# Kernel tuning notes

Measured on AMD Instinct MI355X. Metric: run time of the kernel, lower is better.

The kernel has to match this reference:

```python
import jax, jax.numpy as jnp
import numpy as np

NUM_HEADS = 4
EPS = 1e-5  # GroupNorm default eps


def setup_inputs() -> dict:
    key = jax.random.key(0)
    ks = jax.random.split(key, 4)
    B, T, C, H, W = 4, 8, 128, 96, 96
    x = jax.random.normal(ks[0], (B, T, C, H, W), jnp.float32)
    pos_enc = jax.random.normal(ks[1], (1, 16, C, 1, 1), jnp.float32) * 0.02
    norm_w = jnp.ones((C,), jnp.float32)
    norm_b = jnp.zeros((C,), jnp.float32)
    qkv_w = jax.random.normal(ks[2], (3 * C, C), jnp.float32) * (1.0 / np.sqrt(C))
    proj_w = jax.random.normal(ks[3], (C, C), jnp.float32) * (1.0 / np.sqrt(C))
    return {"x": x, "pos_enc": pos_enc, "norm_w": norm_w, "norm_b": norm_b,
            "qkv_w": qkv_w, "proj_w": proj_w}


def reference(x, pos_enc, norm_w, norm_b, qkv_w, proj_w):
    B, T, C, H, W = x.shape
    nh = NUM_HEADS
    hd = C // nh
    scale = hd ** -0.5

    x = x + pos_enc[:, :T]

    # GroupNorm(1, C): normalize over (C,H,W) per (B,T) sample, biased var
    mean = x.mean(axis=(2, 3, 4), keepdims=True)
    var = x.var(axis=(2, 3, 4), keepdims=True)
    xn = (x - mean) * jax.lax.rsqrt(var + EPS)
    xn = xn * norm_w[None, None, :, None, None] + norm_b[None, None, :, None, None]

    # 1x1 conv -> matmul over channel dim; d = 3C
    qkv = jnp.einsum('btchw,dc->btdhw', xn, qkv_w)
    qkv = qkv.reshape(B, T, 3, nh, hd, H, W)
    q, k, v = qkv[:, :, 0], qkv[:, :, 1], qkv[:, :, 2]  # [B,T,nh,hd,H,W]

    # per-pixel temporal attention: scores [B,nh,H,W,T,T]
    attn = jnp.einsum('btndhw,bsndhw->bnhwts', q, k) * scale
    attn = jax.nn.softmax(attn, axis=-1)

    # only the last query row is kept (out[..., -1, :] in the original)
    out = jnp.einsum('bnhws,bsndhw->bndhw', attn[..., -1, :], v)
    out = out.reshape(B, C, H, W)
    return jnp.einsum('bchw,dc->bdhw', out, proj_w)
```

## Files before the change

kernel.cpp:

```cpp
#include <hip/hip_runtime.h>
#include <math.h>

#define BB 4
#define TT 8
#define CC 128
#define HWW 9216
#define NPG 1179648.0f
#define EPS 1e-5f
#define SCALE 0.17677669529663687f

#define WS_PART 0
#define WS_A    8192
#define WS_B    12288

typedef __attribute__((ext_vector_type(4))) float f32x4;

__device__ __forceinline__ void gload16(const float* g, float* l) {
    __builtin_amdgcn_global_load_lds(
        (const __attribute__((address_space(1))) void*)g,
        (__attribute__((address_space(3))) void*)l,
        16, 0, 0);
}

__global__ __launch_bounds__(256) void stats_kernel(
    const float* __restrict__ x, const float* __restrict__ pe,
    float* __restrict__ part)
{
    const int bid = blockIdx.x;
    const int g = bid >> 7, c = bid & 127;
    const int t = g & 7;
    const int tid = threadIdx.x;
    const float pec = pe[t * CC + c];
    const float4* row = (const float4*)(x + ((size_t)g * CC + c) * HWW);
    float s1 = 0.f, s2 = 0.f;
    #pragma unroll
    for (int i = 0; i < 9; ++i) {
        float4 v = row[tid + i * 256];
        float a = v.x + pec, b = v.y + pec, cc2 = v.z + pec, d = v.w + pec;
        s1 += (a + b) + (cc2 + d);
        s2 += (a * a + b * b) + (cc2 * cc2 + d * d);
    }
    for (int off = 32; off; off >>= 1) {
        s1 += __shfl_down(s1, off);
        s2 += __shfl_down(s2, off);
    }
    __shared__ float red[8];
    const int wid = tid >> 6, lane = tid & 63;
    if (lane == 0) { red[wid] = s1; red[4 + wid] = s2; }
    __syncthreads();
    if (tid == 0) {
        part[bid * 2 + 0] = red[0] + red[1] + red[2] + red[3];
        part[bid * 2 + 1] = red[4] + red[5] + red[6] + red[7];
    }
}

__global__ __launch_bounds__(128) void finalize_kernel(
    const float* __restrict__ pe, const float* __restrict__ nw,
    const float* __restrict__ nb, float* ws)
{
    const int g = blockIdx.x;
    const int c = threadIdx.x;
    const float* part = ws + WS_PART + g * 256;
    float s1 = part[c * 2 + 0];
    float s2 = part[c * 2 + 1];
    for (int off = 32; off; off >>= 1) {
        s1 += __shfl_down(s1, off);
        s2 += __shfl_down(s2, off);
    }
    __shared__ float r[4];
    const int wid = c >> 6, lane = c & 63;
    if (lane == 0) { r[wid] = s1; r[2 + wid] = s2; }
    __syncthreads();
    const float inv = 1.0f / NPG;
    const float mean = (r[0] + r[1]) * inv;
    const float var  = (r[2] + r[3]) * inv - mean * mean;
    const float rstd = rsqrtf(var + EPS);
    const int t = g & 7;
    const float a = rstd * nw[c];
    ws[WS_A + g * CC + c] = a;
    ws[WS_B + g * CC + c] = (pe[t * CC + c] - mean) * a + nb[c];
}

__global__ __launch_bounds__(1024, 4) void fused6_kernel(
    const float* __restrict__ x, const float* __restrict__ ws,
    const float* __restrict__ qkv_w, const float* __restrict__ proj_w,
    float* __restrict__ out)
{
    __shared__ __align__(16) float bufA[CC * 64];
    __shared__ __align__(16) float bufB[CC * 64];

    const int tid  = threadIdx.x;
    const int lane = tid & 63;
    const int w    = tid >> 6;
    const int wu   = __builtin_amdgcn_readfirstlane(w);
    const int n    = wu >> 2;
    const int hq   = wu & 3;
    const int b    = blockIdx.y;
    const int hw0  = blockIdx.x * 64;

    const float* A = ws + WS_A;
    const float* B = ws + WS_B;

    const int rsub = lane >> 4, coff = (lane & 15) * 4;

    auto stage = [&](int t, float* dst) {
        const size_t gb = (size_t)((b * TT + t) * CC) * HWW + hw0 + coff;
        #pragma unroll
        for (int k = 0; k < 2; ++k) {
            const int r0 = wu * 8 + k * 4;
            gload16(x + gb + (size_t)(r0 + rsub) * HWW, dst + r0 * 64);
        }
    };

    float u[32];
    auto score_partial = [&](const float* buf, const float* At, const float* Bt) {
        float s0 = 0.f, s1 = 0.f, s2 = 0.f, s3 = 0.f;
        #pragma unroll
        for (int j = 0; j < 32; j += 4) {
            float x0 = fmaf(buf[(hq * 32 + j + 0) * 64 + lane], At[j + 0], Bt[j + 0]);
            float x1 = fmaf(buf[(hq * 32 + j + 1) * 64 + lane], At[j + 1], Bt[j + 1]);
            float x2 = fmaf(buf[(hq * 32 + j + 2) * 64 + lane], At[j + 2], Bt[j + 2]);
            float x3 = fmaf(buf[(hq * 32 + j + 3) * 64 + lane], At[j + 3], Bt[j + 3]);
            s0 = fmaf(u[j + 0], x0, s0);
            s1 = fmaf(u[j + 1], x1, s1);
            s2 = fmaf(u[j + 2], x2, s2);
            s3 = fmaf(u[j + 3], x3, s3);
        }
        return (s0 + s1) + (s2 + s3);
    };

    stage(7, bufA);
    __syncthreads();

    const int g7 = b * TT + 7;
    const float* A7 = A + g7 * CC;
    const float* B7 = B + g7 * CC;
    {
        const float* Wq = qkv_w + (n * 32 + hq * 8) * CC;
        float q7[8] = {0.f,0.f,0.f,0.f,0.f,0.f,0.f,0.f};
        for (int c0 = 0; c0 < CC; c0 += 8) {
            float xv[8];
            #pragma unroll
            for (int i = 0; i < 8; ++i)
                xv[i] = fmaf(bufA[(c0 + i) * 64 + lane], A7[c0 + i], B7[c0 + i]);
            #pragma unroll
            for (int d = 0; d < 8; ++d) {
                #pragma unroll
                for (int i = 0; i < 8; ++i)
                    q7[d] = fmaf(Wq[d * CC + c0 + i], xv[i], q7[d]);
            }
        }
        #pragma unroll
        for (int d = 0; d < 8; ++d)
            bufB[(n * 32 + hq * 8 + d) * 64 + lane] = q7[d];
    }
    __syncthreads();

    #pragma unroll
    for (int j = 0; j < 32; ++j) u[j] = 0.f;
    {
        const float* Wk = qkv_w + (CC + n * 32) * CC + hq * 32;
        for (int d = 0; d < 32; ++d) {
            const float qv = bufB[(n * 32 + d) * 64 + lane];
            #pragma unroll
            for (int j = 0; j < 32; ++j)
                u[j] = fmaf(Wk[d * CC + j], qv, u[j]);
        }
    }
    __syncthreads();

    float ps[8];
    stage(0, bufB);
    ps[7] = score_partial(bufA, A7 + hq * 32, B7 + hq * 32);
    __syncthreads();
    #pragma unroll
    for (int t = 0; t < 7; ++t) {
        const float* cur = (t & 1) ? bufA : bufB;
        float* oth = (t & 1) ? bufB : bufA;
        if (t < 6) stage(t + 1, oth);
        const float* At = A + (b * TT + t) * CC + hq * 32;
        const float* Bt = B + (b * TT + t) * CC + hq * 32;
        ps[t] = score_partial(cur, At, Bt);
        __syncthreads();
    }

    stage(0, bufB);
    #pragma unroll
    for (int t = 0; t < 8; ++t)
        bufA[(wu * 8 + t) * 64 + lane] = ps[t];
    __syncthreads();

    float wt[8];
    {
        float sreg[8];
        #pragma unroll
        for (int t = 0; t < 8; ++t)
            sreg[t] = (bufA[((n * 4 + 0) * 8 + t) * 64 + lane] +
                       bufA[((n * 4 + 1) * 8 + t) * 64 + lane]) +
                      (bufA[((n * 4 + 2) * 8 + t) * 64 + lane] +
                       bufA[((n * 4 + 3) * 8 + t) * 64 + lane]);
        float m = fmaxf(fmaxf(fmaxf(sreg[0], sreg[1]), fmaxf(sreg[2], sreg[3])),
                        fmaxf(fmaxf(sreg[4], sreg[5]), fmaxf(sreg[6], sreg[7])));
        float l = 0.f;
        #pragma unroll
        for (int t = 0; t < 8; ++t) { wt[t] = __expf((sreg[t] - m) * SCALE); l += wt[t]; }
        const float invl = 1.0f / l;
        #pragma unroll
        for (int t = 0; t < 8; ++t) wt[t] *= invl;
    }
    __syncthreads();

    float xb[32];
    #pragma unroll
    for (int j = 0; j < 32; ++j) xb[j] = 0.f;
    #pragma unroll
    for (int t = 0; t < 8; ++t) {
        const float* cur = (t & 1) ? bufA : bufB;
        float* oth = (t & 1) ? bufB : bufA;
        if (t < 7) stage(t + 1, oth);
        const float* At = A + (b * TT + t) * CC + hq * 32;
        const float* Bt = B + (b * TT + t) * CC + hq * 32;
        const float wc = wt[t];
        #pragma unroll
        for (int j = 0; j < 32; ++j) {
            float xv = fmaf(cur[(hq * 32 + j) * 64 + lane], At[j], Bt[j]);
            xb[j] = fmaf(xv, wc, xb[j]);
        }
        __syncthreads();
    }

    {
        const float* Wv = qkv_w + (2 * CC + n * 32) * CC + hq * 32;
        float vprev[8];
        #pragma unroll
        for (int gi = 0; gi < 4; ++gi) {
            float vp[8];
            #pragma unroll
            for (int d = 0; d < 8; ++d) {
                float s0 = 0.f, s1 = 0.f, s2 = 0.f, s3 = 0.f;
                const float* Wr = Wv + (gi * 8 + d) * CC;
                #pragma unroll
                for (int c = 0; c < 32; c += 4) {
                    s0 = fmaf(Wr[c + 0], xb[c + 0], s0);
                    s1 = fmaf(Wr[c + 1], xb[c + 1], s1);
                    s2 = fmaf(Wr[c + 2], xb[c + 2], s2);
                    s3 = fmaf(Wr[c + 3], xb[c + 3], s3);
                }
                vp[d] = (s0 + s1) + (s2 + s3);
            }
            if (hq == 1) {
                #pragma unroll
                for (int d = 0; d < 8; ++d)
                    bufB[(n * 32 + gi * 8 + d) * 64 + lane] = vp[d];
            }
            if (hq == 3) {
                #pragma unroll
                for (int d = 0; d < 8; ++d)
                    bufA[(n * 32 + gi * 8 + d) * 64 + lane] = vp[d];
            }
            if (gi > 0) {
                if (hq == 0) {
                    #pragma unroll
                    for (int d = 0; d < 8; ++d) {
                        const int r = (n * 32 + (gi - 1) * 8 + d) * 64 + lane;
                        bufB[r] += vprev[d];
                    }
                }
                if (hq == 2) {
                    #pragma unroll
                    for (int d = 0; d < 8; ++d) {
                        const int r = (n * 32 + (gi - 1) * 8 + d) * 64 + lane;
                        bufA[r] += vprev[d];
                    }
                }
            }
            #pragma unroll
            for (int d = 0; d < 8; ++d) vprev[d] = vp[d];
            __syncthreads();
        }
        if (hq == 0) {
            #pragma unroll
            for (int d = 0; d < 8; ++d)
                bufB[(n * 32 + 24 + d) * 64 + lane] += vprev[d];
        }
        if (hq == 2) {
            #pragma unroll
            for (int d = 0; d < 8; ++d)
                bufA[(n * 32 + 24 + d) * 64 + lane] += vprev[d];
        }
    }
    __syncthreads();

    float y[8];
    #pragma unroll
    for (int e = 0; e < 8; ++e) y[e] = 0.f;
    for (int c0 = 0; c0 < CC; c0 += 16) {
        float vv[16];
        #pragma unroll
        for (int i = 0; i < 16; ++i)
            vv[i] = bufB[(c0 + i) * 64 + lane] + bufA[(c0 + i) * 64 + lane];
        #pragma unroll
        for (int e = 0; e < 8; ++e) {
            const float* Pr = proj_w + (wu * 8 + e) * CC + c0;
            #pragma unroll
            for (int i = 0; i < 16; ++i)
                y[e] = fmaf(Pr[i], vv[i], y[e]);
        }
    }
    const size_t ob = (size_t)(b * CC + wu * 8) * HWW + hw0 + lane;
    #pragma unroll
    for (int e = 0; e < 8; ++e)
        out[ob + (size_t)e * HWW] = y[e];
}

extern "C" void kernel_launch(void* const* d_in, const int* in_sizes, int n_in,
                              void* d_out, int out_size, void* d_ws, size_t ws_size,
                              hipStream_t stream) {
    const float* x      = (const float*)d_in[0];
    const float* pe     = (const float*)d_in[1];
    const float* nw     = (const float*)d_in[2];
    const float* nb     = (const float*)d_in[3];
    const float* qkv_w  = (const float*)d_in[4];
    const float* proj_w = (const float*)d_in[5];
    float* out = (float*)d_out;
    float* ws  = (float*)d_ws;

    stats_kernel<<<4096, 256, 0, stream>>>(x, pe, ws + WS_PART);
    finalize_kernel<<<32, 128, 0, stream>>>(pe, nw, nb, ws);
    fused6_kernel<<<dim3(HWW / 64, BB), 1024, 0, stream>>>(x, ws, qkv_w, proj_w, out);
}
```

Measured before the change: 471.6 us.

## Stage x tiles through registers with normalization applied before LDS write

Replaces the direct global-to-LDS async loads with register-staged loads that apply the GroupNorm affine (per-channel a,b held in registers) before writing to shared memory. Consumers then read already-normalized values, removing repeated per-element fma and the scalar loads of A/B coefficients in the score and weighted-sum loops. Loads for tile t+2 are issued ahead so global latency overlaps compute, and the value-accumulation loop is re-pipelined by one step. Softmax switches from __expf to exp2f with a prescaled constant. The cost is more registers per thread and extra VGPR traffic through LDS writes instead of the DMA-style load path.

```diff
diff --git a/kernel.cpp b/kernel.cpp
--- a/kernel.cpp
+++ b/kernel.cpp
@@ -8,19 +8,13 @@
 #define NPG 1179648.0f
 #define EPS 1e-5f
 #define SCALE 0.17677669529663687f
+#define SCALE2 0.2550181765195206f
 
 #define WS_PART 0
 #define WS_A    8192
 #define WS_B    12288
 
 typedef __attribute__((ext_vector_type(4))) float f32x4;
-
-__device__ __forceinline__ void gload16(const float* g, float* l) {
-    __builtin_amdgcn_global_load_lds(
-        (const __attribute__((address_space(1))) void*)g,
-        (__attribute__((address_space(3))) void*)l,
-        16, 0, 0);
-}
 
 __global__ __launch_bounds__(256) void stats_kernel(
     const float* __restrict__ x, const float* __restrict__ pe,
@@ -81,7 +75,7 @@
     ws[WS_B + g * CC + c] = (pe[t * CC + c] - mean) * a + nb[c];
 }
 
-__global__ __launch_bounds__(1024, 4) void fused6_kernel(
+__global__ __launch_bounds__(1024, 4) void fused7_kernel(
     const float* __restrict__ x, const float* __restrict__ ws,
     const float* __restrict__ qkv_w, const float* __restrict__ proj_w,
     float* __restrict__ out)
@@ -98,43 +92,51 @@
     const int b    = blockIdx.y;
     const int hw0  = blockIdx.x * 64;
 
-    const float* A = ws + WS_A;
-    const float* B = ws + WS_B;
-
-    const int rsub = lane >> 4, coff = (lane & 15) * 4;
-
-    auto stage = [&](int t, float* dst) {
-        const size_t gb = (size_t)((b * TT + t) * CC) * HWW + hw0 + coff;
-        #pragma unroll
-        for (int k = 0; k < 2; ++k) {
-            const int r0 = wu * 8 + k * 4;
-            gload16(x + gb + (size_t)(r0 + rsub) * HWW, dst + r0 * 64);
-        }
+    const int r  = tid >> 3;
+    const int k8 = (tid & 7) * 8;
+
+    float ar[8], br[8];
+    #pragma unroll
+    for (int t = 0; t < 8; ++t) {
+        ar[t] = ws[WS_A + (b * TT + t) * CC + r];
+        br[t] = ws[WS_B + (b * TT + t) * CC + r];
+    }
+
+    const float* xrow = x + ((size_t)(b * TT) * CC + r) * HWW + hw0 + k8;
+
+    f32x4 rg0, rg1;
+    auto ldtile = [&](int t) {
+        const float* p = xrow + (size_t)t * CC * HWW;
+        rg0 = *(const f32x4*)(p);
+        rg1 = *(const f32x4*)(p + 4);
     };
+    auto wrtile = [&](float a, float bb2, float* dst) {
+        f32x4 f0, f1;
+        f0.x = fmaf(rg0.x, a, bb2); f0.y = fmaf(rg0.y, a, bb2);
+        f0.z = fmaf(rg0.z, a, bb2); f0.w = fmaf(rg0.w, a, bb2);
+        f1.x = fmaf(rg1.x, a, bb2); f1.y = fmaf(rg1.y, a, bb2);
+        f1.z = fmaf(rg1.z, a, bb2); f1.w = fmaf(rg1.w, a, bb2);
+        *(f32x4*)&dst[r * 64 + k8]     = f0;
+        *(f32x4*)&dst[r * 64 + k8 + 4] = f1;
+    };
 
     float u[32];
-    auto score_partial = [&](const float* buf, const float* At, const float* Bt) {
+    auto score = [&](const float* buf) {
         float s0 = 0.f, s1 = 0.f, s2 = 0.f, s3 = 0.f;
         #pragma unroll
         for (int j = 0; j < 32; j += 4) {
-            float x0 = fmaf(buf[(hq * 32 + j + 0) * 64 + lane], At[j + 0], Bt[j + 0]);
-            float x1 = fmaf(buf[(hq * 32 + j + 1) * 64 + lane], At[j + 1], Bt[j + 1]);
-            float x2 = fmaf(buf[(hq * 32 + j + 2) * 64 + lane], At[j + 2], Bt[j + 2]);
-            float x3 = fmaf(buf[(hq * 32 + j + 3) * 64 + lane], At[j + 3], Bt[j + 3]);
-            s0 = fmaf(u[j + 0], x0, s0);
-            s1 = fmaf(u[j + 1], x1, s1);
-            s2 = fmaf(u[j + 2], x2, s2);
-            s3 = fmaf(u[j + 3], x3, s3);
+            s0 = fmaf(u[j + 0], buf[(hq * 32 + j + 0) * 64 + lane], s0);
+            s1 = fmaf(u[j + 1], buf[(hq * 32 + j + 1) * 64 + lane], s1);
+            s2 = fmaf(u[j + 2], buf[(hq * 32 + j + 2) * 64 + lane], s2);
+            s3 = fmaf(u[j + 3], buf[(hq * 32 + j + 3) * 64 + lane], s3);
         }
         return (s0 + s1) + (s2 + s3);
     };
 
-    stage(7, bufA);
-    __syncthreads();
-
-    const int g7 = b * TT + 7;
-    const float* A7 = A + g7 * CC;
-    const float* B7 = B + g7 * CC;
+    ldtile(7);
+    wrtile(ar[7], br[7], bufA);
+    __syncthreads();
+
     {
         const float* Wq = qkv_w + (n * 32 + hq * 8) * CC;
         float q7[8] = {0.f,0.f,0.f,0.f,0.f,0.f,0.f,0.f};
@@ -142,7 +144,7 @@
             float xv[8];
             #pragma unroll
             for (int i = 0; i < 8; ++i)
-                xv[i] = fmaf(bufA[(c0 + i) * 64 + lane], A7[c0 + i], B7[c0 + i]);
+                xv[i] = bufA[(c0 + i) * 64 + lane];
             #pragma unroll
             for (int d = 0; d < 8; ++d) {
                 #pragma unroll
@@ -156,6 +158,8 @@
     }
     __syncthreads();
 
+    ldtile(0);
+
     #pragma unroll
     for (int j = 0; j < 32; ++j) u[j] = 0.f;
     {
@@ -170,21 +174,29 @@
     __syncthreads();
 
     float ps[8];
-    stage(0, bufB);
-    ps[7] = score_partial(bufA, A7 + hq * 32, B7 + hq * 32);
-    __syncthreads();
+    wrtile(ar[0], br[0], bufB);
+    ps[7] = score(bufA);
+    ldtile(1);
+    __syncthreads();
+
     #pragma unroll
     for (int t = 0; t < 7; ++t) {
-        const float* cur = (t & 1) ? bufA : bufB;
-        float* oth = (t & 1) ? bufB : bufA;
-        if (t < 6) stage(t + 1, oth);
-        const float* At = A + (b * TT + t) * CC + hq * 32;
-        const float* Bt = B + (b * TT + t) * CC + hq * 32;
-        ps[t] = score_partial(cur, At, Bt);
+        const float* curb = (t & 1) ? bufA : bufB;
+        float* othb = (t & 1) ? bufB : bufA;
+        if (t < 6) {
+            if (t == 0) wrtile(ar[1], br[1], othb);
+            if (t == 1) wrtile(ar[2], br[2], othb);
+            if (t == 2) wrtile(ar[3], br[3], othb);
+            if (t == 3) wrtile(ar[4], br[4], othb);
+            if (t == 4) wrtile(ar[5], br[5], othb);
+            if (t == 5) wrtile(ar[6], br[6], othb);
+        }
+        if (t < 5) ldtile(t + 2);
+        ps[t] = score(curb);
         __syncthreads();
     }
 
-    stage(0, bufB);
+    ldtile(0);
     #pragma unroll
     for (int t = 0; t < 8; ++t)
         bufA[(wu * 8 + t) * 64 + lane] = ps[t];
@@ -203,7 +215,7 @@
                         fmaxf(fmaxf(sreg[4], sreg[5]), fmaxf(sreg[6], sreg[7])));
         float l = 0.f;
         #pragma unroll
-        for (int t = 0; t < 8; ++t) { wt[t] = __expf((sreg[t] - m) * SCALE); l += wt[t]; }
+        for (int t = 0; t < 8; ++t) { wt[t] = exp2f((sreg[t] - m) * SCALE2); l += wt[t]; }
         const float invl = 1.0f / l;
         #pragma unroll
         for (int t = 0; t < 8; ++t) wt[t] *= invl;
@@ -215,19 +227,34 @@
     for (int j = 0; j < 32; ++j) xb[j] = 0.f;
     #pragma unroll
     for (int t = 0; t < 8; ++t) {
-        const float* cur = (t & 1) ? bufA : bufB;
-        float* oth = (t & 1) ? bufB : bufA;
-        if (t < 7) stage(t + 1, oth);
-        const float* At = A + (b * TT + t) * CC + hq * 32;
-        const float* Bt = B + (b * TT + t) * CC + hq * 32;
-        const float wc = wt[t];
-        #pragma unroll
-        for (int j = 0; j < 32; ++j) {
-            float xv = fmaf(cur[(hq * 32 + j) * 64 + lane], At[j], Bt[j]);
-            xb[j] = fmaf(xv, wc, xb[j]);
+        float* wb = (t & 1) ? bufB : bufA;
+        {
+            if (t == 0) wrtile(ar[0], br[0], wb);
+            if (t == 1) wrtile(ar[1], br[1], wb);
+            if (t == 2) wrtile(ar[2], br[2], wb);
+            if (t == 3) wrtile(ar[3], br[3], wb);
+            if (t == 4) wrtile(ar[4], br[4], wb);
+            if (t == 5) wrtile(ar[5], br[5], wb);
+            if (t == 6) wrtile(ar[6], br[6], wb);
+            if (t == 7) wrtile(ar[7], br[7], wb);
+        }
+        if (t < 7) ldtile(t + 1);
+        if (t >= 1) {
+            const float* rb = (t & 1) ? bufA : bufB;
+            const float wc = wt[t - 1];
+            #pragma unroll
+            for (int j = 0; j < 32; ++j)
+                xb[j] = fmaf(rb[(hq * 32 + j) * 64 + lane], wc, xb[j]);
         }
         __syncthreads();
     }
+    {
+        const float wc = wt[7];
+        #pragma unroll
+        for (int j = 0; j < 32; ++j)
+            xb[j] = fmaf(bufB[(hq * 32 + j) * 64 + lane], wc, xb[j]);
+    }
+    __syncthreads();
 
     {
         const float* Wv = qkv_w + (2 * CC + n * 32) * CC + hq * 32;
@@ -261,17 +288,13 @@
             if (gi > 0) {
                 if (hq == 0) {
                     #pragma unroll
-                    for (int d = 0; d < 8; ++d) {
-                        const int r = (n * 32 + (gi - 1) * 8 + d) * 64 + lane;
-                        bufB[r] += vprev[d];
-                    }
+                    for (int d = 0; d < 8; ++d)
+                        bufB[(n * 32 + (gi - 1) * 8 + d) * 64 + lane] += vprev[d];
                 }
                 if (hq == 2) {
                     #pragma unroll
-                    for (int d = 0; d < 8; ++d) {
-                        const int r = (n * 32 + (gi - 1) * 8 + d) * 64 + lane;
-                        bufA[r] += vprev[d];
-                    }
+                    for (int d = 0; d < 8; ++d)
+                        bufA[(n * 32 + (gi - 1) * 8 + d) * 64 + lane] += vprev[d];
                 }
             }
             #pragma unroll
@@ -327,5 +350,5 @@
 
     stats_kernel<<<4096, 256, 0, stream>>>(x, pe, ws + WS_PART);
     finalize_kernel<<<32, 128, 0, stream>>>(pe, nw, nb, ws);
-    fused6_kernel<<<dim3(HWW / 64, BB), 1024, 0, stream>>>(x, ws, qkv_w, proj_w, out);
+    fused7_kernel<<<dim3(HWW / 64, BB), 1024, 0, stream>>>(x, ws, qkv_w, proj_w, out);
 }
```

Measured after the change: 413.9 us. 1.14x faster.
